# Kernel optimization log

Hardware: AMD Instinct MI355X
Metric: run time of the kernel (lower is better)

Reference implementation:

```python
import jax, jax.numpy as jnp
import numpy as np

N_NODES = 100000
N_EDGES = 1600000
DIM = 64


def setup_inputs() -> dict:
    key = jax.random.key(0)
    k1, k2, k3 = jax.random.split(key, 3)
    x = jax.random.normal(k1, (N_NODES, DIM), dtype=jnp.float32)
    edge_index = jax.random.randint(k2, (2, N_EDGES), 0, N_NODES, dtype=jnp.int64)
    W = jax.random.normal(k3, (DIM, DIM), dtype=jnp.float32) * (1.0 / np.sqrt(DIM))
    b = jnp.zeros((DIM,), dtype=jnp.float32)
    return {"x": x, "edge_index": edge_index, "W": W, "b": b}


def reference(x, edge_index, W, b):
    # GCNConv (PyG defaults): add self-loops, symmetric normalization,
    # linear transform, scatter-add aggregation, bias; then ReLU.
    N = x.shape[0]
    loop = jnp.arange(N, dtype=edge_index.dtype)
    row = jnp.concatenate([edge_index[0], loop])  # source nodes
    col = jnp.concatenate([edge_index[1], loop])  # target nodes
    ew = jnp.ones(row.shape[0], dtype=x.dtype)

    deg = jax.ops.segment_sum(ew, col, num_segments=N)  # [N]
    dinv = jnp.where(deg > 0, jax.lax.rsqrt(deg), 0.0)
    norm = dinv[row] * ew * dinv[col]  # [E+N]

    xw = x @ W.T  # [N, D] small GEMM
    msg = norm[:, None] * xw[row]  # gather + scale, [E+N, D]
    out = jax.ops.segment_sum(msg, col, num_segments=N) + b  # scatter-add
    return jax.nn.relu(out)
```

## Files before the change

### kernel.cpp

```cpp
#include <hip/hip_runtime.h>
#include <hip/hip_bf16.h>

#define N_NODES 100000
#define N_EDGES 1600000
#define DIM 64
#define NBUCK 782
#define BK_NODES 128
#define CAP 2560
#define HA_EPB 4096
#define HA_BLOCKS 391

typedef unsigned int uint32;
typedef __attribute__((ext_vector_type(8))) short bf16x8;
typedef __attribute__((ext_vector_type(4))) float f32x4;

__device__ __forceinline__ float bflo(uint32 u) { return __uint_as_float(u << 16); }
__device__ __forceinline__ float bfhi(uint32 u) { return __uint_as_float(u & 0xffff0000u); }

__device__ __forceinline__ short f2bf(float f) {
    __hip_bfloat16 h = __float2bfloat16(f);
    return (short)__builtin_bit_cast(unsigned short, h);
}
__device__ __forceinline__ uint32 pack2bf(float lo, float hi) {
    unsigned short a = __builtin_bit_cast(unsigned short, __float2bfloat16(lo));
    unsigned short b = __builtin_bit_cast(unsigned short, __float2bfloat16(hi));
    return ((uint32)b << 16) | (uint32)a;
}

__global__ __launch_bounds__(1024) void zero_kernel(int* __restrict__ bcnt) {
    if (threadIdx.x < NBUCK) bcnt[threadIdx.x] = 0;
}

__global__ __launch_bounds__(1024) void scatter_kernel(const int* __restrict__ row,
                                                       const int* __restrict__ col,
                                                       int* __restrict__ bcnt,
                                                       int* __restrict__ pairs) {
    __shared__ int h[NBUCK];
    __shared__ int base[NBUCK];
    if (threadIdx.x < NBUCK) h[threadIdx.x] = 0;
    __syncthreads();

    const int bstart = blockIdx.x * HA_EPB;
    int r[4], c[4];
#pragma unroll 4
    for (int k = 0; k < 4; ++k) {
        int e = bstart + threadIdx.x + k * 1024;
        if (e < N_EDGES) {
            r[k] = row[e];
            c[k] = col[e];
            atomicAdd(&h[c[k] >> 7], 1);
        }
    }
    __syncthreads();
    if (threadIdx.x < NBUCK) {
        int v = h[threadIdx.x];
        base[threadIdx.x] = v ? atomicAdd(&bcnt[threadIdx.x], v) : 0;
        h[threadIdx.x] = 0;
    }
    __syncthreads();
#pragma unroll 4
    for (int k = 0; k < 4; ++k) {
        int e = bstart + threadIdx.x + k * 1024;
        if (e < N_EDGES) {
            int bk = c[k] >> 7;
            int pos = base[bk] + atomicAdd(&h[bk], 1);
            if (pos < CAP) pairs[bk * CAP + pos] = (r[k] << 7) | (c[k] & 127);
        }
    }
}

__global__ __launch_bounds__(256) void sort_kernel(const int* __restrict__ bcnt,
                                                   int* __restrict__ pairs,
                                                   int* __restrict__ info,
                                                   float* __restrict__ dinv) {
    __shared__ int cnt[BK_NODES];
    __shared__ int sc[BK_NODES];
    __shared__ int cur[BK_NODES];
    __shared__ int buf[CAP];
    const int b = blockIdx.x;
    const int tid = threadIdx.x;
    const int n = bcnt[b];
    if (tid < BK_NODES) cnt[tid] = 0;
    __syncthreads();
    for (int p = tid; p < n; p += 256) {
        int pk = pairs[b * CAP + p];
        buf[p] = pk;
        atomicAdd(&cnt[pk & 127], 1);
    }
    __syncthreads();
    if (tid < BK_NODES) {
        int lane = tid & 63;
        int sum = cnt[tid];
#pragma unroll
        for (int d = 1; d < 64; d <<= 1) {
            int t = __shfl_up(sum, d);
            if (lane >= d) sum += t;
        }
        sc[tid] = sum;
    }
    __syncthreads();
    if (tid >= 64 && tid < BK_NODES) sc[tid] += sc[63];
    __syncthreads();
    if (tid < BK_NODES) {
        int ex = sc[tid] - cnt[tid];
        cur[tid] = ex;
        int node = b * BK_NODES + tid;
        if (node < N_NODES) {
            info[node] = ((b * CAP + ex) << 8) | cnt[tid];
            dinv[node] = rsqrtf((float)(cnt[tid] + 1));
        }
    }
    __syncthreads();
    for (int p = tid; p < n; p += 256) {
        int pk = buf[p];
        int pos = atomicAdd(&cur[pk & 127], 1);
        pairs[b * CAP + pos] = pk >> 7;
    }
}

__global__ __launch_bounds__(256) void gemm_kernel(const float* __restrict__ x,
                                                   const float* __restrict__ W,
                                                   const float* __restrict__ dinv,
                                                   uint32* __restrict__ sbw) {
    __shared__ float lds[64 * 64];
    const int wave = threadIdx.x >> 6;
    const int lane = threadIdx.x & 63;
    const int base = blockIdx.x * 64;
    const int r16 = lane & 15;
    const int kb = lane >> 4;

    bf16x8 wb[4][2];
#pragma unroll
    for (int t = 0; t < 4; ++t) {
#pragma unroll
        for (int h = 0; h < 2; ++h) {
            const float* wp = &W[(r16 + 16 * t) * DIM + 32 * h + kb * 8];
            float4 p0 = *(const float4*)wp;
            float4 p1 = *(const float4*)(wp + 4);
            bf16x8 f;
            f[0] = f2bf(p0.x); f[1] = f2bf(p0.y); f[2] = f2bf(p0.z); f[3] = f2bf(p0.w);
            f[4] = f2bf(p1.x); f[5] = f2bf(p1.y); f[6] = f2bf(p1.z); f[7] = f2bf(p1.w);
            wb[t][h] = f;
        }
    }

    int arow = base + wave * 16 + r16;
    if (arow >= N_NODES) arow = N_NODES - 1;
    bf16x8 af[2];
#pragma unroll
    for (int h = 0; h < 2; ++h) {
        const float* xp = &x[(size_t)arow * DIM + 32 * h + kb * 8];
        float4 p0 = *(const float4*)xp;
        float4 p1 = *(const float4*)(xp + 4);
        bf16x8 f;
        f[0] = f2bf(p0.x); f[1] = f2bf(p0.y); f[2] = f2bf(p0.z); f[3] = f2bf(p0.w);
        f[4] = f2bf(p1.x); f[5] = f2bf(p1.y); f[6] = f2bf(p1.z); f[7] = f2bf(p1.w);
        af[h] = f;
    }

    float dv[4];
#pragma unroll
    for (int i = 0; i < 4; ++i) {
        int rr = base + wave * 16 + kb * 4 + i;
        dv[i] = dinv[rr < N_NODES ? rr : N_NODES - 1];
    }

#pragma unroll
    for (int t = 0; t < 4; ++t) {
        f32x4 c = {0.0f, 0.0f, 0.0f, 0.0f};
        c = __builtin_amdgcn_mfma_f32_16x16x32_bf16(af[0], wb[t][0], c, 0, 0, 0);
        c = __builtin_amdgcn_mfma_f32_16x16x32_bf16(af[1], wb[t][1], c, 0, 0, 0);
#pragma unroll
        for (int i = 0; i < 4; ++i)
            lds[(wave * 16 + kb * 4 + i) * 64 + r16 + 16 * t] = c[i] * dv[i];
    }
    __syncthreads();

    int r = threadIdx.x >> 2;
    int cb = threadIdx.x & 3;
    int nrow = base + r;
    if (nrow < N_NODES) {
        const float* src = &lds[r * 64 + cb * 16];
        uint32 o[8];
#pragma unroll
        for (int j = 0; j < 8; ++j) {
            float2 f = *(const float2*)&src[2 * j];
            o[j] = pack2bf(f.x, f.y);
        }
        uint32* dst = sbw + (size_t)nrow * 32 + cb * 8;
        *(uint4*)dst = make_uint4(o[0], o[1], o[2], o[3]);
        *(uint4*)(dst + 4) = make_uint4(o[4], o[5], o[6], o[7]);
    }
}

__global__ __launch_bounds__(256) void agg_kernel(const int* __restrict__ info,
                                                  const int* __restrict__ srow,
                                                  const uint2* __restrict__ s4,
                                                  const float* __restrict__ dinv,
                                                  const float* __restrict__ bias,
                                                  float* __restrict__ out) {
    int n = __builtin_amdgcn_readfirstlane(blockIdx.x * 4 + (threadIdx.x >> 6));
    if (n >= N_NODES) return;
    const int lane = threadIdx.x & 63;
    const int q = lane >> 4;
    const int l = lane & 15;

    const int iv = info[n];
    const int start = iv >> 8;
    const int end = start + (iv & 255);

    float a0 = 0.0f, a1 = 0.0f, a2 = 0.0f, a3 = 0.0f;
    int p = start + q;
    for (; p + 12 < end; p += 16) {
        int r0 = srow[p];
        int r1 = srow[p + 4];
        int r2 = srow[p + 8];
        int r3 = srow[p + 12];
        uint2 u0 = s4[(size_t)r0 * 16 + l];
        uint2 u1 = s4[(size_t)r1 * 16 + l];
        uint2 u2 = s4[(size_t)r2 * 16 + l];
        uint2 u3 = s4[(size_t)r3 * 16 + l];
        a0 += bflo(u0.x); a1 += bfhi(u0.x); a2 += bflo(u0.y); a3 += bfhi(u0.y);
        a0 += bflo(u1.x); a1 += bfhi(u1.x); a2 += bflo(u1.y); a3 += bfhi(u1.y);
        a0 += bflo(u2.x); a1 += bfhi(u2.x); a2 += bflo(u2.y); a3 += bfhi(u2.y);
        a0 += bflo(u3.x); a1 += bfhi(u3.x); a2 += bflo(u3.y); a3 += bfhi(u3.y);
    }
    for (; p < end; p += 4) {
        int r0 = srow[p];
        uint2 u0 = s4[(size_t)r0 * 16 + l];
        a0 += bflo(u0.x); a1 += bfhi(u0.x); a2 += bflo(u0.y); a3 += bfhi(u0.y);
    }

    a0 += __shfl_xor(a0, 16); a1 += __shfl_xor(a1, 16);
    a2 += __shfl_xor(a2, 16); a3 += __shfl_xor(a3, 16);
    a0 += __shfl_xor(a0, 32); a1 += __shfl_xor(a1, 32);
    a2 += __shfl_xor(a2, 32); a3 += __shfl_xor(a3, 32);

    if (lane < 16) {
        uint2 us = s4[(size_t)n * 16 + l];
        a0 += bflo(us.x); a1 += bfhi(us.x); a2 += bflo(us.y); a3 += bfhi(us.y);
        float4 bb = *(const float4*)&bias[4 * l];
        float d = dinv[n];
        float4 o;
        o.x = fmaxf(fmaf(d, a0, bb.x), 0.0f);
        o.y = fmaxf(fmaf(d, a1, bb.y), 0.0f);
        o.z = fmaxf(fmaf(d, a2, bb.z), 0.0f);
        o.w = fmaxf(fmaf(d, a3, bb.w), 0.0f);
        *(float4*)&out[(size_t)n * DIM + 4 * l] = o;
    }
}

extern "C" void kernel_launch(void* const* d_in, const int* in_sizes, int n_in,
                              void* d_out, int out_size, void* d_ws, size_t ws_size,
                              hipStream_t stream) {
    const float* x    = (const float*)d_in[0];
    const int*   ei   = (const int*)d_in[1];
    const float* W    = (const float*)d_in[2];
    const float* bias = (const float*)d_in[3];
    float*       out  = (float*)d_out;

    const int* row = ei;
    const int* col = ei + N_EDGES;

    char* ws = (char*)d_ws;
    int*    bcnt  = (int*)(ws + 0);
    int*    info  = (int*)(ws + 4096);
    float*  dinv  = (float*)(ws + 404224);
    int*    pairs = (int*)(ws + 804352);
    uint32* sbw   = (uint32*)(ws + 8812160);

    zero_kernel<<<1, 1024, 0, stream>>>(bcnt);
    scatter_kernel<<<HA_BLOCKS, 1024, 0, stream>>>(row, col, bcnt, pairs);
    sort_kernel<<<NBUCK, 256, 0, stream>>>(bcnt, pairs, info, dinv);
    gemm_kernel<<<(N_NODES + 63) / 64, 256, 0, stream>>>(x, W, dinv, sbw);
    agg_kernel<<<(N_NODES + 3) / 4, 256, 0, stream>>>(info, pairs, (const uint2*)sbw,
                                                      dinv, bias, out);
}
```

Before: 107.3 us.

## Split feature table into two halves and aggregate each half separately

The GEMM output is now written as two separate bf16 tables, one per 32-column half, and the aggregation grid gains a second dimension so each block gathers only one half. Each half-table is half the size of the old one, so its working set is more likely to stay cached during the random gathers. The cost is twice as many index reads and blocks. Separately, the scatter kernel now processes 16K edges per block instead of 4K, which cuts global bucket atomics but leaves fewer blocks to fill the GPU.

```diff
diff --git a/kernel.cpp b/kernel.cpp
--- a/kernel.cpp
+++ b/kernel.cpp
@@ -7,8 +7,8 @@
 #define NBUCK 782
 #define BK_NODES 128
 #define CAP 2560
-#define HA_EPB 4096
-#define HA_BLOCKS 391
+#define HA_EPB 16384
+#define HA_BLOCKS 98
 
 typedef unsigned int uint32;
 typedef __attribute__((ext_vector_type(8))) short bf16x8;
@@ -41,9 +41,9 @@
     __syncthreads();
 
     const int bstart = blockIdx.x * HA_EPB;
-    int r[4], c[4];
-#pragma unroll 4
-    for (int k = 0; k < 4; ++k) {
+    int r[16], c[16];
+#pragma unroll 16
+    for (int k = 0; k < 16; ++k) {
         int e = bstart + threadIdx.x + k * 1024;
         if (e < N_EDGES) {
             r[k] = row[e];
@@ -58,8 +58,8 @@
         h[threadIdx.x] = 0;
     }
     __syncthreads();
-#pragma unroll 4
-    for (int k = 0; k < 4; ++k) {
+#pragma unroll 16
+    for (int k = 0; k < 16; ++k) {
         int e = bstart + threadIdx.x + k * 1024;
         if (e < N_EDGES) {
             int bk = c[k] >> 7;
@@ -121,7 +121,8 @@
 __global__ __launch_bounds__(256) void gemm_kernel(const float* __restrict__ x,
                                                    const float* __restrict__ W,
                                                    const float* __restrict__ dinv,
-                                                   uint32* __restrict__ sbw) {
+                                                   uint32* __restrict__ sbA,
+                                                   uint32* __restrict__ sbB) {
     __shared__ float lds[64 * 64];
     const int wave = threadIdx.x >> 6;
     const int lane = threadIdx.x & 63;
@@ -187,7 +188,8 @@
             float2 f = *(const float2*)&src[2 * j];
             o[j] = pack2bf(f.x, f.y);
         }
-        uint32* dst = sbw + (size_t)nrow * 32 + cb * 8;
+        uint32* dst = (cb < 2) ? (sbA + (size_t)nrow * 16 + cb * 8)
+                               : (sbB + (size_t)nrow * 16 + (cb - 2) * 8);
         *(uint4*)dst = make_uint4(o[0], o[1], o[2], o[3]);
         *(uint4*)(dst + 4) = make_uint4(o[4], o[5], o[6], o[7]);
     }
@@ -195,58 +197,57 @@
 
 __global__ __launch_bounds__(256) void agg_kernel(const int* __restrict__ info,
                                                   const int* __restrict__ srow,
-                                                  const uint2* __restrict__ s4,
+                                                  const uint2* __restrict__ sA,
+                                                  const uint2* __restrict__ sB,
                                                   const float* __restrict__ dinv,
                                                   const float* __restrict__ bias,
                                                   float* __restrict__ out) {
+    const int half = blockIdx.y;
     int n = __builtin_amdgcn_readfirstlane(blockIdx.x * 4 + (threadIdx.x >> 6));
     if (n >= N_NODES) return;
+    const uint2* __restrict__ s4 = half ? sB : sA;
     const int lane = threadIdx.x & 63;
-    const int q = lane >> 4;
-    const int l = lane & 15;
+    const int slot = lane >> 3;
+    const int l = lane & 7;
 
     const int iv = info[n];
     const int start = iv >> 8;
     const int end = start + (iv & 255);
 
     float a0 = 0.0f, a1 = 0.0f, a2 = 0.0f, a3 = 0.0f;
-    int p = start + q;
-    for (; p + 12 < end; p += 16) {
+    int p = start + slot;
+    for (; p + 8 < end; p += 16) {
         int r0 = srow[p];
-        int r1 = srow[p + 4];
-        int r2 = srow[p + 8];
-        int r3 = srow[p + 12];
-        uint2 u0 = s4[(size_t)r0 * 16 + l];
-        uint2 u1 = s4[(size_t)r1 * 16 + l];
-        uint2 u2 = s4[(size_t)r2 * 16 + l];
-        uint2 u3 = s4[(size_t)r3 * 16 + l];
+        int r1 = srow[p + 8];
+        uint2 u0 = s4[(size_t)r0 * 8 + l];
+        uint2 u1 = s4[(size_t)r1 * 8 + l];
         a0 += bflo(u0.x); a1 += bfhi(u0.x); a2 += bflo(u0.y); a3 += bfhi(u0.y);
         a0 += bflo(u1.x); a1 += bfhi(u1.x); a2 += bflo(u1.y); a3 += bfhi(u1.y);
-        a0 += bflo(u2.x); a1 += bfhi(u2.x); a2 += bflo(u2.y); a3 += bfhi(u2.y);
-        a0 += bflo(u3.x); a1 += bfhi(u3.x); a2 += bflo(u3.y); a3 += bfhi(u3.y);
-    }
-    for (; p < end; p += 4) {
+    }
+    if (p < end) {
         int r0 = srow[p];
-        uint2 u0 = s4[(size_t)r0 * 16 + l];
+        uint2 u0 = s4[(size_t)r0 * 8 + l];
         a0 += bflo(u0.x); a1 += bfhi(u0.x); a2 += bflo(u0.y); a3 += bfhi(u0.y);
     }
 
+    a0 += __shfl_xor(a0, 8);  a1 += __shfl_xor(a1, 8);
+    a2 += __shfl_xor(a2, 8);  a3 += __shfl_xor(a3, 8);
     a0 += __shfl_xor(a0, 16); a1 += __shfl_xor(a1, 16);
     a2 += __shfl_xor(a2, 16); a3 += __shfl_xor(a3, 16);
     a0 += __shfl_xor(a0, 32); a1 += __shfl_xor(a1, 32);
     a2 += __shfl_xor(a2, 32); a3 += __shfl_xor(a3, 32);
 
-    if (lane < 16) {
-        uint2 us = s4[(size_t)n * 16 + l];
+    if (lane < 8) {
+        uint2 us = s4[(size_t)n * 8 + l];
         a0 += bflo(us.x); a1 += bfhi(us.x); a2 += bflo(us.y); a3 += bfhi(us.y);
-        float4 bb = *(const float4*)&bias[4 * l];
+        float4 bb = *(const float4*)&bias[half * 32 + 4 * l];
         float d = dinv[n];
         float4 o;
         o.x = fmaxf(fmaf(d, a0, bb.x), 0.0f);
         o.y = fmaxf(fmaf(d, a1, bb.y), 0.0f);
         o.z = fmaxf(fmaf(d, a2, bb.z), 0.0f);
         o.w = fmaxf(fmaf(d, a3, bb.w), 0.0f);
-        *(float4*)&out[(size_t)n * DIM + 4 * l] = o;
+        *(float4*)&out[(size_t)n * DIM + half * 32 + 4 * l] = o;
     }
 }
 
@@ -267,12 +268,14 @@
     int*    info  = (int*)(ws + 4096);
     float*  dinv  = (float*)(ws + 404224);
     int*    pairs = (int*)(ws + 804352);
-    uint32* sbw   = (uint32*)(ws + 8812160);
+    uint32* sbA   = (uint32*)(ws + 8812160);
+    uint32* sbB   = (uint32*)(ws + 15212288);
 
     zero_kernel<<<1, 1024, 0, stream>>>(bcnt);
     scatter_kernel<<<HA_BLOCKS, 1024, 0, stream>>>(row, col, bcnt, pairs);
     sort_kernel<<<NBUCK, 256, 0, stream>>>(bcnt, pairs, info, dinv);
-    gemm_kernel<<<(N_NODES + 63) / 64, 256, 0, stream>>>(x, W, dinv, sbw);
-    agg_kernel<<<(N_NODES + 3) / 4, 256, 0, stream>>>(info, pairs, (const uint2*)sbw,
-                                                      dinv, bias, out);
-}
+    gemm_kernel<<<(N_NODES + 63) / 64, 256, 0, stream>>>(x, W, dinv, sbA, sbB);
+    dim3 agrid((N_NODES + 3) / 4, 2);
+    agg_kernel<<<agrid, 256, 0, stream>>>(info, pairs, (const uint2*)sbA,
+                                          (const uint2*)sbB, dinv, bias, out);
+}
```

Result: slower. 128.9 us (+20.1%).

## Fuse sort and GEMM kernels, move source normalization into aggregation

Applied to the files above, without the earlier changes.

The GEMM no longer scales its rows by dinv, which removes its dependency on the sort, so sort and GEMM run as one launch with blocks picking a role by index and sharing a union of LDS buffers. The aggregation now loads dinv for each source row and applies it with FMAs, and the output is written with nontemporal stores. The scatter kernel handles four times as many edges per block using fewer blocks, and the zero kernel is replaced by hipMemsetAsync. In exchange, agg does an extra random gather per edge and the scatter kernel uses more registers with less parallelism.

```diff
diff --git a/kernel.cpp b/kernel.cpp
--- a/kernel.cpp
+++ b/kernel.cpp
@@ -7,8 +7,9 @@
 #define NBUCK 782
 #define BK_NODES 128
 #define CAP 2560
-#define HA_EPB 4096
-#define HA_BLOCKS 391
+#define HA_EPB 16384
+#define HA_BLOCKS 98
+#define GEMM_BLOCKS 1563
 
 typedef unsigned int uint32;
 typedef __attribute__((ext_vector_type(8))) short bf16x8;
@@ -25,10 +26,6 @@
     unsigned short a = __builtin_bit_cast(unsigned short, __float2bfloat16(lo));
     unsigned short b = __builtin_bit_cast(unsigned short, __float2bfloat16(hi));
     return ((uint32)b << 16) | (uint32)a;
-}
-
-__global__ __launch_bounds__(1024) void zero_kernel(int* __restrict__ bcnt) {
-    if (threadIdx.x < NBUCK) bcnt[threadIdx.x] = 0;
 }
 
 __global__ __launch_bounds__(1024) void scatter_kernel(const int* __restrict__ row,
@@ -41,9 +38,9 @@
     __syncthreads();
 
     const int bstart = blockIdx.x * HA_EPB;
-    int r[4], c[4];
-#pragma unroll 4
-    for (int k = 0; k < 4; ++k) {
+    int r[16], c[16];
+#pragma unroll 16
+    for (int k = 0; k < 16; ++k) {
         int e = bstart + threadIdx.x + k * 1024;
         if (e < N_EDGES) {
             r[k] = row[e];
@@ -58,8 +55,8 @@
         h[threadIdx.x] = 0;
     }
     __syncthreads();
-#pragma unroll 4
-    for (int k = 0; k < 4; ++k) {
+#pragma unroll 16
+    for (int k = 0; k < 16; ++k) {
         int e = bstart + threadIdx.x + k * 1024;
         if (e < N_EDGES) {
             int bk = c[k] >> 7;
@@ -69,127 +66,129 @@
     }
 }
 
-__global__ __launch_bounds__(256) void sort_kernel(const int* __restrict__ bcnt,
-                                                   int* __restrict__ pairs,
-                                                   int* __restrict__ info,
-                                                   float* __restrict__ dinv) {
-    __shared__ int cnt[BK_NODES];
-    __shared__ int sc[BK_NODES];
-    __shared__ int cur[BK_NODES];
-    __shared__ int buf[CAP];
-    const int b = blockIdx.x;
+struct SortSmem {
+    int cnt[BK_NODES];
+    int sc[BK_NODES];
+    int cur[BK_NODES];
+    int buf[CAP];
+};
+union FusedSmem {
+    SortSmem s;
+    float g[64 * 64];
+};
+
+__global__ __launch_bounds__(256) void sortgemm_kernel(const int* __restrict__ bcnt,
+                                                       int* __restrict__ pairs,
+                                                       int* __restrict__ info,
+                                                       float* __restrict__ dinv,
+                                                       const float* __restrict__ x,
+                                                       const float* __restrict__ W,
+                                                       uint32* __restrict__ sbw) {
+    __shared__ FusedSmem u;
     const int tid = threadIdx.x;
-    const int n = bcnt[b];
-    if (tid < BK_NODES) cnt[tid] = 0;
-    __syncthreads();
-    for (int p = tid; p < n; p += 256) {
-        int pk = pairs[b * CAP + p];
-        buf[p] = pk;
-        atomicAdd(&cnt[pk & 127], 1);
-    }
-    __syncthreads();
-    if (tid < BK_NODES) {
-        int lane = tid & 63;
-        int sum = cnt[tid];
-#pragma unroll
-        for (int d = 1; d < 64; d <<= 1) {
-            int t = __shfl_up(sum, d);
-            if (lane >= d) sum += t;
-        }
-        sc[tid] = sum;
-    }
-    __syncthreads();
-    if (tid >= 64 && tid < BK_NODES) sc[tid] += sc[63];
-    __syncthreads();
-    if (tid < BK_NODES) {
-        int ex = sc[tid] - cnt[tid];
-        cur[tid] = ex;
-        int node = b * BK_NODES + tid;
-        if (node < N_NODES) {
-            info[node] = ((b * CAP + ex) << 8) | cnt[tid];
-            dinv[node] = rsqrtf((float)(cnt[tid] + 1));
-        }
-    }
-    __syncthreads();
-    for (int p = tid; p < n; p += 256) {
-        int pk = buf[p];
-        int pos = atomicAdd(&cur[pk & 127], 1);
-        pairs[b * CAP + pos] = pk >> 7;
-    }
-}
-
-__global__ __launch_bounds__(256) void gemm_kernel(const float* __restrict__ x,
-                                                   const float* __restrict__ W,
-                                                   const float* __restrict__ dinv,
-                                                   uint32* __restrict__ sbw) {
-    __shared__ float lds[64 * 64];
-    const int wave = threadIdx.x >> 6;
-    const int lane = threadIdx.x & 63;
-    const int base = blockIdx.x * 64;
-    const int r16 = lane & 15;
-    const int kb = lane >> 4;
-
-    bf16x8 wb[4][2];
-#pragma unroll
-    for (int t = 0; t < 4; ++t) {
+
+    if (blockIdx.x < NBUCK) {
+        const int b = blockIdx.x;
+        int n = bcnt[b];
+        if (n > CAP) n = CAP;
+        if (tid < BK_NODES) u.s.cnt[tid] = 0;
+        __syncthreads();
+        for (int p = tid; p < n; p += 256) {
+            int pk = pairs[b * CAP + p];
+            u.s.buf[p] = pk;
+            atomicAdd(&u.s.cnt[pk & 127], 1);
+        }
+        __syncthreads();
+        if (tid < BK_NODES) {
+            int lane = tid & 63;
+            int sum = u.s.cnt[tid];
+#pragma unroll
+            for (int d = 1; d < 64; d <<= 1) {
+                int t = __shfl_up(sum, d);
+                if (lane >= d) sum += t;
+            }
+            u.s.sc[tid] = sum;
+        }
+        __syncthreads();
+        if (tid >= 64 && tid < BK_NODES) u.s.sc[tid] += u.s.sc[63];
+        __syncthreads();
+        if (tid < BK_NODES) {
+            int ex = u.s.sc[tid] - u.s.cnt[tid];
+            u.s.cur[tid] = ex;
+            int node = b * BK_NODES + tid;
+            if (node < N_NODES) {
+                info[node] = ((b * CAP + ex) << 8) | u.s.cnt[tid];
+                dinv[node] = rsqrtf((float)(u.s.cnt[tid] + 1));
+            }
+        }
+        __syncthreads();
+        for (int p = tid; p < n; p += 256) {
+            int pk = u.s.buf[p];
+            int pos = atomicAdd(&u.s.cur[pk & 127], 1);
+            pairs[b * CAP + pos] = pk >> 7;
+        }
+    } else {
+        const int wave = tid >> 6;
+        const int lane = tid & 63;
+        const int base = (blockIdx.x - NBUCK) * 64;
+        const int r16 = lane & 15;
+        const int kb = lane >> 4;
+
+        bf16x8 wb[4][2];
+#pragma unroll
+        for (int t = 0; t < 4; ++t) {
+#pragma unroll
+            for (int h = 0; h < 2; ++h) {
+                const float* wp = &W[(r16 + 16 * t) * DIM + 32 * h + kb * 8];
+                float4 p0 = *(const float4*)wp;
+                float4 p1 = *(const float4*)(wp + 4);
+                bf16x8 f;
+                f[0] = f2bf(p0.x); f[1] = f2bf(p0.y); f[2] = f2bf(p0.z); f[3] = f2bf(p0.w);
+                f[4] = f2bf(p1.x); f[5] = f2bf(p1.y); f[6] = f2bf(p1.z); f[7] = f2bf(p1.w);
+                wb[t][h] = f;
+            }
+        }
+
+        int arow = base + wave * 16 + r16;
+        if (arow >= N_NODES) arow = N_NODES - 1;
+        bf16x8 af[2];
 #pragma unroll
         for (int h = 0; h < 2; ++h) {
-            const float* wp = &W[(r16 + 16 * t) * DIM + 32 * h + kb * 8];
-            float4 p0 = *(const float4*)wp;
-            float4 p1 = *(const float4*)(wp + 4);
+            const float* xp = &x[(size_t)arow * DIM + 32 * h + kb * 8];
+            float4 p0 = *(const float4*)xp;
+            float4 p1 = *(const float4*)(xp + 4);
             bf16x8 f;
             f[0] = f2bf(p0.x); f[1] = f2bf(p0.y); f[2] = f2bf(p0.z); f[3] = f2bf(p0.w);
             f[4] = f2bf(p1.x); f[5] = f2bf(p1.y); f[6] = f2bf(p1.z); f[7] = f2bf(p1.w);
-            wb[t][h] = f;
-        }
-    }
-
-    int arow = base + wave * 16 + r16;
-    if (arow >= N_NODES) arow = N_NODES - 1;
-    bf16x8 af[2];
-#pragma unroll
-    for (int h = 0; h < 2; ++h) {
-        const float* xp = &x[(size_t)arow * DIM + 32 * h + kb * 8];
-        float4 p0 = *(const float4*)xp;
-        float4 p1 = *(const float4*)(xp + 4);
-        bf16x8 f;
-        f[0] = f2bf(p0.x); f[1] = f2bf(p0.y); f[2] = f2bf(p0.z); f[3] = f2bf(p0.w);
-        f[4] = f2bf(p1.x); f[5] = f2bf(p1.y); f[6] = f2bf(p1.z); f[7] = f2bf(p1.w);
-        af[h] = f;
-    }
-
-    float dv[4];
-#pragma unroll
-    for (int i = 0; i < 4; ++i) {
-        int rr = base + wave * 16 + kb * 4 + i;
-        dv[i] = dinv[rr < N_NODES ? rr : N_NODES - 1];
-    }
-
-#pragma unroll
-    for (int t = 0; t < 4; ++t) {
-        f32x4 c = {0.0f, 0.0f, 0.0f, 0.0f};
-        c = __builtin_amdgcn_mfma_f32_16x16x32_bf16(af[0], wb[t][0], c, 0, 0, 0);
-        c = __builtin_amdgcn_mfma_f32_16x16x32_bf16(af[1], wb[t][1], c, 0, 0, 0);
-#pragma unroll
-        for (int i = 0; i < 4; ++i)
-            lds[(wave * 16 + kb * 4 + i) * 64 + r16 + 16 * t] = c[i] * dv[i];
-    }
-    __syncthreads();
-
-    int r = threadIdx.x >> 2;
-    int cb = threadIdx.x & 3;
-    int nrow = base + r;
-    if (nrow < N_NODES) {
-        const float* src = &lds[r * 64 + cb * 16];
-        uint32 o[8];
-#pragma unroll
-        for (int j = 0; j < 8; ++j) {
-            float2 f = *(const float2*)&src[2 * j];
-            o[j] = pack2bf(f.x, f.y);
-        }
-        uint32* dst = sbw + (size_t)nrow * 32 + cb * 8;
-        *(uint4*)dst = make_uint4(o[0], o[1], o[2], o[3]);
-        *(uint4*)(dst + 4) = make_uint4(o[4], o[5], o[6], o[7]);
+            af[h] = f;
+        }
+
+#pragma unroll
+        for (int t = 0; t < 4; ++t) {
+            f32x4 c = {0.0f, 0.0f, 0.0f, 0.0f};
+            c = __builtin_amdgcn_mfma_f32_16x16x32_bf16(af[0], wb[t][0], c, 0, 0, 0);
+            c = __builtin_amdgcn_mfma_f32_16x16x32_bf16(af[1], wb[t][1], c, 0, 0, 0);
+#pragma unroll
+            for (int i = 0; i < 4; ++i)
+                u.g[(wave * 16 + kb * 4 + i) * 64 + r16 + 16 * t] = c[i];
+        }
+        __syncthreads();
+
+        int r = tid >> 2;
+        int cb = tid & 3;
+        int nrow = base + r;
+        if (nrow < N_NODES) {
+            const float* src = &u.g[r * 64 + cb * 16];
+            uint32 o[8];
+#pragma unroll
+            for (int j = 0; j < 8; ++j) {
+                float2 f = *(const float2*)&src[2 * j];
+                o[j] = pack2bf(f.x, f.y);
+            }
+            uint32* dst = sbw + (size_t)nrow * 32 + cb * 8;
+            *(uint4*)dst = make_uint4(o[0], o[1], o[2], o[3]);
+            *(uint4*)(dst + 4) = make_uint4(o[4], o[5], o[6], o[7]);
+        }
     }
 }
 
@@ -216,19 +215,26 @@
         int r1 = srow[p + 4];
         int r2 = srow[p + 8];
         int r3 = srow[p + 12];
+        float d0 = dinv[r0], d1 = dinv[r1], d2 = dinv[r2], d3 = dinv[r3];
         uint2 u0 = s4[(size_t)r0 * 16 + l];
         uint2 u1 = s4[(size_t)r1 * 16 + l];
         uint2 u2 = s4[(size_t)r2 * 16 + l];
         uint2 u3 = s4[(size_t)r3 * 16 + l];
-        a0 += bflo(u0.x); a1 += bfhi(u0.x); a2 += bflo(u0.y); a3 += bfhi(u0.y);
-        a0 += bflo(u1.x); a1 += bfhi(u1.x); a2 += bflo(u1.y); a3 += bfhi(u1.y);
-        a0 += bflo(u2.x); a1 += bfhi(u2.x); a2 += bflo(u2.y); a3 += bfhi(u2.y);
-        a0 += bflo(u3.x); a1 += bfhi(u3.x); a2 += bflo(u3.y); a3 += bfhi(u3.y);
+        a0 = fmaf(d0, bflo(u0.x), a0); a1 = fmaf(d0, bfhi(u0.x), a1);
+        a2 = fmaf(d0, bflo(u0.y), a2); a3 = fmaf(d0, bfhi(u0.y), a3);
+        a0 = fmaf(d1, bflo(u1.x), a0); a1 = fmaf(d1, bfhi(u1.x), a1);
+        a2 = fmaf(d1, bflo(u1.y), a2); a3 = fmaf(d1, bfhi(u1.y), a3);
+        a0 = fmaf(d2, bflo(u2.x), a0); a1 = fmaf(d2, bfhi(u2.x), a1);
+        a2 = fmaf(d2, bflo(u2.y), a2); a3 = fmaf(d2, bfhi(u2.y), a3);
+        a0 = fmaf(d3, bflo(u3.x), a0); a1 = fmaf(d3, bfhi(u3.x), a1);
+        a2 = fmaf(d3, bflo(u3.y), a2); a3 = fmaf(d3, bfhi(u3.y), a3);
     }
     for (; p < end; p += 4) {
         int r0 = srow[p];
+        float d0 = dinv[r0];
         uint2 u0 = s4[(size_t)r0 * 16 + l];
-        a0 += bflo(u0.x); a1 += bfhi(u0.x); a2 += bflo(u0.y); a3 += bfhi(u0.y);
+        a0 = fmaf(d0, bflo(u0.x), a0); a1 = fmaf(d0, bfhi(u0.x), a1);
+        a2 = fmaf(d0, bflo(u0.y), a2); a3 = fmaf(d0, bfhi(u0.y), a3);
     }
 
     a0 += __shfl_xor(a0, 16); a1 += __shfl_xor(a1, 16);
@@ -237,16 +243,17 @@
     a2 += __shfl_xor(a2, 32); a3 += __shfl_xor(a3, 32);
 
     if (lane < 16) {
+        float dc = dinv[n];
         uint2 us = s4[(size_t)n * 16 + l];
-        a0 += bflo(us.x); a1 += bfhi(us.x); a2 += bflo(us.y); a3 += bfhi(us.y);
+        a0 = fmaf(dc, bflo(us.x), a0); a1 = fmaf(dc, bfhi(us.x), a1);
+        a2 = fmaf(dc, bflo(us.y), a2); a3 = fmaf(dc, bfhi(us.y), a3);
         float4 bb = *(const float4*)&bias[4 * l];
-        float d = dinv[n];
-        float4 o;
-        o.x = fmaxf(fmaf(d, a0, bb.x), 0.0f);
-        o.y = fmaxf(fmaf(d, a1, bb.y), 0.0f);
-        o.z = fmaxf(fmaf(d, a2, bb.z), 0.0f);
-        o.w = fmaxf(fmaf(d, a3, bb.w), 0.0f);
-        *(float4*)&out[(size_t)n * DIM + 4 * l] = o;
+        f32x4 o;
+        o[0] = fmaxf(fmaf(dc, a0, bb.x), 0.0f);
+        o[1] = fmaxf(fmaf(dc, a1, bb.y), 0.0f);
+        o[2] = fmaxf(fmaf(dc, a2, bb.z), 0.0f);
+        o[3] = fmaxf(fmaf(dc, a3, bb.w), 0.0f);
+        __builtin_nontemporal_store(o, (f32x4*)&out[(size_t)n * DIM + 4 * l]);
     }
 }
 
@@ -269,10 +276,10 @@
     int*    pairs = (int*)(ws + 804352);
     uint32* sbw   = (uint32*)(ws + 8812160);
 
-    zero_kernel<<<1, 1024, 0, stream>>>(bcnt);
+    hipMemsetAsync(bcnt, 0, 4096, stream);
     scatter_kernel<<<HA_BLOCKS, 1024, 0, stream>>>(row, col, bcnt, pairs);
-    sort_kernel<<<NBUCK, 256, 0, stream>>>(bcnt, pairs, info, dinv);
-    gemm_kernel<<<(N_NODES + 63) / 64, 256, 0, stream>>>(x, W, dinv, sbw);
+    sortgemm_kernel<<<NBUCK + GEMM_BLOCKS, 256, 0, stream>>>(bcnt, pairs, info, dinv,
+                                                             x, W, sbw);
     agg_kernel<<<(N_NODES + 3) / 4, 256, 0, stream>>>(info, pairs, (const uint2*)sbw,
                                                       dinv, bias, out);
 }
```

Measured after the change: 103.9 us. 1.03x faster.
